# Kernel optimization log

Measured on AMD Instinct MI355X. Metric: run time of the kernel, lower is better.

## Reference

```python
import jax, jax.numpy as jnp
import numpy as np

B, S, D, H, DH = 2, 1024, 1024, 16, 64
SCALE = 1.0 / np.sqrt(DH)


def setup_inputs() -> dict:
    key = jax.random.key(0)
    ks = jax.random.split(key, 9)
    return {
        "x": jax.random.normal(ks[0], (B, S, D), jnp.float32),
        "qkv_w": jax.random.normal(ks[1], (3 * H * DH, D), jnp.float32) * 0.02,
        "out_w": jax.random.normal(ks[2], (D, H * DH), jnp.float32) * 0.02,
        "bias_p": jax.random.uniform(ks[3], (H, 1, 1), jnp.float32) * 2.0,
        "bias_a": jax.random.uniform(ks[4], (H, 1, 1), jnp.float32),
        "mlp_w1": jax.random.normal(ks[5], (H, 2 * H), jnp.float32) * 0.1,
        "mlp_b1": jnp.zeros((H,), jnp.float32),
        "mlp_w2": jax.random.normal(ks[6], (H, H), jnp.float32) * 0.1,
        "mlp_b2": jnp.zeros((H,), jnp.float32),
    }


def reference(x, qkv_w, out_w, bias_p, bias_a, mlp_w1, mlp_b1, mlp_w2, mlp_b2):
    # qkv projection: torch Linear => x @ W.T
    qkv = (x @ qkv_w.T).reshape(B, S, 3, H, DH)
    q = qkv[:, :, 0].transpose(0, 2, 1, 3)  # [B,H,S,DH]
    k = qkv[:, :, 1].transpose(0, 2, 1, 3)
    v = qkv[:, :, 2].transpose(0, 2, 1, 3)

    scores = jnp.einsum('bhqd,bhkd->bhqk', q, k) * SCALE  # [B,H,S,S]

    # Kerple additive bias: -p * log1p(a * |i-j|), per head
    p = jnp.clip(bias_p, 0.01)
    a = jnp.clip(bias_a, 0.01)
    pos = jnp.arange(S, dtype=jnp.float32)
    dist = jnp.abs(pos[None, :] - pos[:, None])  # [S,S]
    kb = -p * jnp.log1p(a * dist)  # [H,S,S]

    # DAPE refinement MLP over per-(i,j) head features
    z = jnp.concatenate(
        [scores, jnp.broadcast_to(kb[None], (B, H, S, S))], axis=1
    ).transpose(0, 2, 3, 1)  # [B,S,S,2H]
    hdn = jax.nn.gelu(z @ mlp_w1.T + mlp_b1, approximate=False)  # [B,S,S,H]
    refine = (hdn @ mlp_w2.T + mlp_b2).transpose(0, 3, 1, 2)  # [B,H,S,S]

    scores = scores + kb[None] + refine
    attn = jax.nn.softmax(scores, axis=-1)  # dropout is identity in eval

    out = jnp.einsum('bhqk,bhkd->bhqd', attn, v)  # [B,H,S,DH]
    out = out.transpose(0, 2, 1, 3).reshape(B, S, H * DH)
    return out @ out_w.T
```

## Files before the change

### kernel.cpp

```cpp
#include <hip/hip_runtime.h>
#include <math.h>

#define Bsz 2
#define Ssz 1024
#define Dsz 1024
#define Hn 16
#define DHsz 64
#define QKV3 3072
#define SCALE 0.125f

typedef __bf16 bf16;
typedef bf16 bf16x8 __attribute__((ext_vector_type(8)));
typedef bf16 bf16x4 __attribute__((ext_vector_type(4)));
typedef float f32x4 __attribute__((ext_vector_type(4)));

#define MFMA(a, b, c) __builtin_amdgcn_mfma_f32_16x16x32_bf16(a, b, c, 0, 0, 0)
#define LDT 72

#define SCSLAB(b, i, c) \
  ((size_t)(b) * 16777216 + (size_t)(i) * 16384 + (size_t)(c) * 4096)

__global__ void cast_all(const float* __restrict__ x, const float* __restrict__ qw,
                         const float* __restrict__ ow, bf16* __restrict__ xh,
                         bf16* __restrict__ wh, bf16* __restrict__ owh) {
  int idx = (blockIdx.x * 256 + threadIdx.x) * 4;
  const float* src;
  bf16* dst;
  int off = idx;
  if (idx < 2097152) {
    src = x; dst = xh;
  } else if (idx < 2097152 + 3145728) {
    src = qw; dst = wh; off = idx - 2097152;
  } else {
    src = ow; dst = owh; off = idx - (2097152 + 3145728);
  }
  float4 v = *(const float4*)(src + off);
  bf16x4 hv = {(bf16)v.x, (bf16)v.y, (bf16)v.z, (bf16)v.w};
  *(bf16x4*)(dst + off) = hv;
}

__global__ void tk_wfrag(const float* __restrict__ bias_p, const float* __restrict__ bias_a,
                         const float* __restrict__ w1, const float* __restrict__ b1,
                         const float* __restrict__ w2, float2* __restrict__ tk,
                         bf16* __restrict__ wf) {
  if (blockIdx.x == 128) {
    int lane = threadIdx.x;
    if (lane < 64) {
      int l15 = lane & 15, q8 = (lane >> 4) << 3;
      bf16x8 w1d, w2a;
#pragma unroll
      for (int e = 0; e < 8; ++e) {
        int k = q8 + e;
        if (k < 16) {
          w1d[e] = (bf16)w1[l15 * 32 + k];
        } else {
          float w = w1[l15 * 32 + k - 16];
          w1d[e] = (bf16)(w - (float)(bf16)w);
        }
        w2a[e] = (bf16)w2[l15 * 16 + (k & 15)];
      }
      *(bf16x8*)(wf + lane * 8) = w1d;
      *(bf16x8*)(wf + 512 + lane * 8) = w2a;
    }
    return;
  }
  int idx = blockIdx.x * 256 + threadIdx.x;
  int o = idx >> 4, n = idx & 15;
  int d = o - 1024; if (d < 0) d = -d; if (d > 1023) d = 1023;
  float fd = (float)d;
  float t1 = b1[n];
  float t2 = 0.f;
#pragma unroll
  for (int h = 0; h < 16; ++h) {
    float kb = -fmaxf(bias_p[h], 0.01f) * log1pf(fmaxf(bias_a[h], 0.01f) * fd);
    t1 += w1[n * 32 + 16 + h] * kb;
    if (h == n) t2 = kb;
  }
  tk[idx] = make_float2(t1, t2);
}

__global__ __launch_bounds__(256, 3) void k1_qkv(const bf16* __restrict__ A,
                                                 const bf16* __restrict__ B,
                                                 bf16* __restrict__ C) {
  __shared__ __align__(16) bf16 sA[128 * LDT];
  __shared__ __align__(16) bf16 sB[96 * LDT];
  const int tid = threadIdx.x;
  const int lane = tid & 63, wv = tid >> 6;
  const int wr = wv >> 1, wc = wv & 1;
  const int l15 = lane & 15, q8 = (lane >> 4) << 3, q4 = (lane >> 4) << 2;
  const int m0 = blockIdx.y * 128, n0 = blockIdx.x * 96;
  const int r0 = tid >> 3, c8 = (tid & 7) << 3;

  f32x4 acc[4][3];
#pragma unroll
  for (int t = 0; t < 4; ++t)
#pragma unroll
    for (int u = 0; u < 3; ++u)
#pragma unroll
      for (int r = 0; r < 4; ++r) acc[t][u][r] = 0.f;

  bf16x8 rA[4], rB[3];
#define K1_LOAD(kt)                                                         \
  {                                                                         \
    _Pragma("unroll") for (int c = 0; c < 4; ++c)                           \
      rA[c] = *(const bf16x8*)(A + (size_t)(m0 + c * 32 + r0) * Dsz + (kt) + c8);  \
    _Pragma("unroll") for (int c = 0; c < 3; ++c)                           \
      rB[c] = *(const bf16x8*)(B + (size_t)(n0 + c * 32 + r0) * Dsz + (kt) + c8);  \
  }

  K1_LOAD(0)
  for (int kt = 0; kt < Dsz; kt += 64) {
    __syncthreads();
#pragma unroll
    for (int c = 0; c < 4; ++c) *(bf16x8*)&sA[(c * 32 + r0) * LDT + c8] = rA[c];
#pragma unroll
    for (int c = 0; c < 3; ++c) *(bf16x8*)&sB[(c * 32 + r0) * LDT + c8] = rB[c];
    __syncthreads();
    if (kt + 64 < Dsz) K1_LOAD(kt + 64)
#pragma unroll
    for (int ks = 0; ks < 64; ks += 32) {
      bf16x8 fa[4], fb[3];
#pragma unroll
      for (int t = 0; t < 4; ++t)
        fa[t] = *(const bf16x8*)&sA[(wr * 64 + t * 16 + l15) * LDT + ks + q8];
#pragma unroll
      for (int u = 0; u < 3; ++u)
        fb[u] = *(const bf16x8*)&sB[(wc * 48 + u * 16 + l15) * LDT + ks + q8];
#pragma unroll
      for (int t = 0; t < 4; ++t)
#pragma unroll
        for (int u = 0; u < 3; ++u) acc[t][u] = MFMA(fa[t], fb[u], acc[t][u]);
    }
  }
#undef K1_LOAD

#define K1BST 104
  bf16* sBounce = sA;
#pragma unroll
  for (int t = 0; t < 4; ++t) {
    __syncthreads();
#pragma unroll
    for (int u = 0; u < 3; ++u) {
      int col = wc * 48 + u * 16 + l15;
#pragma unroll
      for (int r = 0; r < 4; ++r)
        sBounce[(wr * 16 + q4 + r) * K1BST + col] = (bf16)acc[t][u][r];
    }
    __syncthreads();
    int lr = tid >> 3;
    int grow = m0 + (lr < 16 ? t * 16 + lr : 64 + t * 16 + (lr - 16));
#pragma unroll
    for (int cg = 0; cg < 3; ++cg) {
      int cc = cg * 32 + (tid & 7) * 4;
      bf16x4 vv = *(const bf16x4*)&sBounce[lr * K1BST + cc];
      *(bf16x4*)(C + (size_t)grow * QKV3 + n0 + cc) = vv;
    }
  }
#undef K1BST
}

__global__ void pack_vt(const bf16* __restrict__ qkv, bf16* __restrict__ vt) {
  __shared__ __align__(16) bf16 T[64 * LDT];
  const int tid = threadIdx.x;
  const int bh = blockIdx.y, b = bh >> 4, h = bh & 15;
  const int j0 = blockIdx.x * 64;
#pragma unroll
  for (int c = 0; c < 2; ++c) {
    int lin = c * 256 + tid;
    int jr = lin >> 3, d8 = (lin & 7) << 3;
    bf16x8 v = *(const bf16x8*)(qkv + (size_t)(b * Ssz + j0 + jr) * QKV3 + 2048 + h * DHsz + d8);
#pragma unroll
    for (int e = 0; e < 8; ++e) T[(d8 + e) * LDT + jr] = v[e];
  }
  __syncthreads();
#pragma unroll
  for (int c = 0; c < 2; ++c) {
    int lin = c * 256 + tid;
    int d = lin >> 3, j8 = (lin & 7) << 3;
    bf16x8 o = *(const bf16x8*)&T[d * LDT + j8];
    *(bf16x8*)(vt + ((size_t)(b * Hn + h) * DHsz + d) * Ssz + j0 + j8) = o;
  }
}

__global__ __launch_bounds__(256, 3) void k2_qk(const bf16* __restrict__ qkv,
                                                bf16* __restrict__ scores) {
  __shared__ __align__(16) bf16 sA[128 * LDT], sB[128 * LDT];
  const int tid = threadIdx.x;
  const int lane = tid & 63, wv = tid >> 6;
  const int wr = wv >> 1, wc = wv & 1;
  const int l15 = lane & 15, q8 = (lane >> 4) << 3, q4 = (lane >> 4) << 2;
  const int z = blockIdx.z, b = z >> 4, h = z & 15;
  const int i0 = blockIdx.y * 128, j0 = blockIdx.x * 128;
  const bf16* Ab = qkv + (size_t)b * Ssz * QKV3 + h * DHsz;
  const bf16* Bb = Ab + Ssz;
  const int r0 = tid >> 3, c8 = (tid & 7) << 3;
#pragma unroll
  for (int c = 0; c < 4; ++c) {
    int row = c * 32 + r0;
    *(bf16x8*)&sA[row * LDT + c8] = *(const bf16x8*)(Ab + (size_t)(i0 + row) * QKV3 + c8);
    *(bf16x8*)&sB[row * LDT + c8] = *(const bf16x8*)(Bb + (size_t)(j0 + row) * QKV3 + c8);
  }
  __syncthreads();
  f32x4 acc[4][4];
#pragma unroll
  for (int t = 0; t < 4; ++t)
#pragma unroll
    for (int u = 0; u < 4; ++u)
#pragma unroll
      for (int r = 0; r < 4; ++r) acc[t][u][r] = 0.f;
#pragma unroll
  for (int ks = 0; ks < 64; ks += 32) {
    bf16x8 fa[4], fb[4];
#pragma unroll
    for (int t = 0; t < 4; ++t) fa[t] = *(const bf16x8*)&sA[(wr * 64 + t * 16 + l15) * LDT + ks + q8];
#pragma unroll
    for (int u = 0; u < 4; ++u) fb[u] = *(const bf16x8*)&sB[(wc * 64 + u * 16 + l15) * LDT + ks + q8];
#pragma unroll
    for (int t = 0; t < 4; ++t)
#pragma unroll
      for (int u = 0; u < 4; ++u) acc[t][u] = MFMA(fa[t], fb[u], acc[t][u]);
  }

#define K2BST 136
  bf16* sBounce = sA;
  const int chnk = j0 >> 8, jhalf = j0 & 128;
  bf16* base2 = scores + SCSLAB(b, 0, chnk) + h * 256 + jhalf;
#pragma unroll
  for (int t = 0; t < 4; ++t) {
    __syncthreads();
#pragma unroll
    for (int u = 0; u < 4; ++u) {
      int col = wc * 64 + u * 16 + l15;
#pragma unroll
      for (int r = 0; r < 4; ++r)
        sBounce[(wr * 16 + q4 + r) * K2BST + col] = (bf16)(acc[t][u][r] * SCALE);
    }
    __syncthreads();
#pragma unroll
    for (int hf = 0; hf < 2; ++hf) {
      int lr = hf * 16 + (tid >> 4);
      int cc = (tid & 15) * 8;
      bf16x8 vv = *(const bf16x8*)&sBounce[lr * K2BST + cc];
      int grow = i0 + (lr < 16 ? t * 16 + lr : 64 + t * 16 + (lr - 16));
      *(bf16x8*)(base2 + (size_t)grow * 16384 + cc) = vv;
    }
  }
#undef K2BST
}

__device__ __forceinline__ float gelu_fast(float x) {
  float z = fabsf(x) * 0.70710678118654752f;
  float t = __builtin_amdgcn_rcpf(fmaf(0.47047f, z, 1.0f));
  float poly = t * fmaf(t, fmaf(t, 0.7478556f, -0.0958798f), 0.3480242f);
  float erfa = 1.0f - poly * __expf(-z * z);
  float erfs = copysignf(erfa, x);
  return 0.5f * x * (1.0f + erfs);
}

#define SHS 264

__global__ __launch_bounds__(256, 8) void dape_softmax(bf16* scores,
                                                       const float2* __restrict__ tk,
                                                       const bf16* __restrict__ wf,
                                                       const float* __restrict__ b2,
                                                       float* __restrict__ sums) {
  const int c = blockIdx.x;
  const int i = blockIdx.y;
  const int b = blockIdx.z;
  const int tid = threadIdx.x;
  const int lane = tid & 63, wv = tid >> 6;
  const int l15 = lane & 15, q = lane >> 4;
  const int q8 = q << 3, q4 = q << 2;

  __shared__ bf16 sH[Hn][SHS];
  __shared__ __align__(16) bf16 hdnS[4][2][16][40];
  __shared__ float sumLDS[4][16];

  const bf16x8 w1d = *(const bf16x8*)(wf + lane * 8);
  const bf16x8 w2a = *(const bf16x8*)(wf + 512 + lane * 8);
  const float bias2 = b2[l15];

  if (lane < 32) {
    int row = lane >> 1, col = 16 + (lane & 1) * 8;
    *(bf16x8*)&hdnS[wv][0][row][col] = (bf16x8){};
    *(bf16x8*)&hdnS[wv][1][row][col] = (bf16x8){};
  }

  const int jw = wv * 64;
  bf16* slab = scores + SCSLAB(b, i, c);
#pragma unroll
  for (int t = 0; t < 2; ++t) {
    int h = t * 8 + (lane >> 3);
    int col = jw + (lane & 7) * 8;
    *(bf16x8*)&sH[h][col] = *(const bf16x8*)(slab + h * 256 + col);
  }

  const float2* tkp = tk + ((size_t)(c * 256 + jw + q4 - i + 1024) << 4) + l15;
  bf16* prow = slab + l15 * 256 + jw;
  float psum = 0.f;

#pragma unroll
  for (int jt = 0; jt < 4; ++jt) {
    const int j0c = jw + jt * 16;
    bf16x8 a1;
#pragma unroll
    for (int e = 0; e < 8; ++e) a1[e] = sH[(q8 + e) & 15][j0c + l15];
    float2 tkv[4];
#pragma unroll
    for (int r = 0; r < 4; ++r) tkv[r] = tkp[jt * 256 + r * 16];
    f32x4 c1 = {tkv[0].x, tkv[1].x, tkv[2].x, tkv[3].x};
    c1 = MFMA(a1, w1d, c1);
#pragma unroll
    for (int r = 0; r < 4; ++r) hdnS[wv][jt & 1][q4 + r][l15] = (bf16)gelu_fast(c1[r]);
    bf16x8 a2 = *(const bf16x8*)&hdnS[wv][jt & 1][l15][q8];
    f32x4 c2 = {bias2, bias2, bias2, bias2};
    c2 = MFMA(a2, w2a, c2);
    bf16x4 sc4 = *(const bf16x4*)&sH[l15][j0c + q4];
    f32x4 pv;
#pragma unroll
    for (int r = 0; r < 4; ++r) {
      float lg = (float)sc4[r] + tkv[r].y + c2[r];
      pv[r] = __expf(lg);
      psum += pv[r];
    }
    bf16x4 p4 = {(bf16)pv[0], (bf16)pv[1], (bf16)pv[2], (bf16)pv[3]};
    *(bf16x4*)(prow + jt * 16 + q4) = p4;
  }

  psum += __shfl_xor(psum, 16, 64);
  psum += __shfl_xor(psum, 32, 64);
  if (lane < 16) sumLDS[wv][lane] = psum;
  __syncthreads();
  if (tid < 16) {
    float tot = sumLDS[0][tid] + sumLDS[1][tid] + sumLDS[2][tid] + sumLDS[3][tid];
    sums[((((b << 10) + i) << 4) + tid) * 4 + c] = tot;
  }
}

__global__ __launch_bounds__(256, 6) void k4_av(const bf16* __restrict__ attn,
                                                const bf16* __restrict__ vt,
                                                const float* __restrict__ sums,
                                                bf16* __restrict__ aout) {
  __shared__ __align__(16) bf16 sA[64 * LDT], sB[64 * LDT];
  const int tid = threadIdx.x;
  const int lane = tid & 63, wv = tid >> 6;
  const int wr = wv >> 1, wc = wv & 1;
  const int l15 = lane & 15, q8 = (lane >> 4) << 3, q4 = (lane >> 4) << 2;
  const int i0 = blockIdx.x * 64, h = blockIdx.y, b = blockIdx.z;
  const bf16* Ab = attn + SCSLAB(b, i0, 0) + h * 256;
  const bf16* Bb = vt + (size_t)(b * Hn + h) * DHsz * Ssz;
  const int r0 = tid >> 3, c8 = (tid & 7) << 3;
  f32x4 acc[2][2];
#pragma unroll
  for (int t = 0; t < 2; ++t)
#pragma unroll
    for (int u = 0; u < 2; ++u)
#pragma unroll
      for (int r = 0; r < 4; ++r) acc[t][u][r] = 0.f;
  bf16x8 rA[2], rB[2];
#define K4_LOAD(kt)                                                          \
  {                                                                          \
    _Pragma("unroll") for (int c = 0; c < 2; ++c) {                          \
      int row = c * 32 + r0;                                                 \
      rA[c] = *(const bf16x8*)(Ab + (size_t)row * 16384 +                    \
                               (((kt) >> 8) * 4096) + ((kt) & 255) + c8);    \
      rB[c] = *(const bf16x8*)(Bb + ((size_t)row << 10) + (kt) + c8);        \
    }                                                                        \
  }
  K4_LOAD(0)
  for (int kt = 0; kt < Ssz; kt += 64) {
    __syncthreads();
#pragma unroll
    for (int c = 0; c < 2; ++c) {
      int row = c * 32 + r0;
      *(bf16x8*)&sA[row * LDT + c8] = rA[c];
      *(bf16x8*)&sB[row * LDT + c8] = rB[c];
    }
    __syncthreads();
    if (kt + 64 < Ssz) K4_LOAD(kt + 64)
#pragma unroll
    for (int ks = 0; ks < 64; ks += 32) {
      bf16x8 fa[2], fb[2];
#pragma unroll
      for (int t = 0; t < 2; ++t) fa[t] = *(const bf16x8*)&sA[(wr * 32 + t * 16 + l15) * LDT + ks + q8];
#pragma unroll
      for (int u = 0; u < 2; ++u) fb[u] = *(const bf16x8*)&sB[(wc * 32 + u * 16 + l15) * LDT + ks + q8];
#pragma unroll
      for (int t = 0; t < 2; ++t)
#pragma unroll
        for (int u = 0; u < 2; ++u) acc[t][u] = MFMA(fa[t], fb[u], acc[t][u]);
    }
  }
#undef K4_LOAD

  bf16* sBounce = sA;
  __syncthreads();
#pragma unroll
  for (int t = 0; t < 2; ++t)
#pragma unroll
    for (int r = 0; r < 4; ++r) {
      int lr = wr * 32 + t * 16 + q4 + r;
      int row = i0 + lr;
      f32x4 sv = *(const f32x4*)&sums[((((b << 10) + row) << 4) + h) * 4];
      float inv = 1.f / (sv[0] + sv[1] + sv[2] + sv[3]);
#pragma unroll
      for (int u = 0; u < 2; ++u)
        sBounce[lr * LDT + wc * 32 + u * 16 + l15] = (bf16)(acc[t][u][r] * inv);
    }
  __syncthreads();
#pragma unroll
  for (int r2 = 0; r2 < 2; ++r2) {
    int lr = r2 * 32 + (tid >> 3);
    int cc = (tid & 7) * 8;
    bf16x8 vv = *(const bf16x8*)&sBounce[lr * LDT + cc];
    *(bf16x8*)(aout + (size_t)(b * Ssz + i0 + lr) * Dsz + h * DHsz + cc) = vv;
  }
}

__global__ __launch_bounds__(256, 6) void k5_out(const bf16* __restrict__ A,
                                                 const bf16* __restrict__ B,
                                                 float* __restrict__ C) {
  __shared__ __align__(16) bf16 sA[64 * LDT], sB[64 * LDT];
  const int tid = threadIdx.x;
  const int lane = tid & 63, wv = tid >> 6;
  const int wr = wv >> 1, wc = wv & 1;
  const int l15 = lane & 15, q8 = (lane >> 4) << 3, q4 = (lane >> 4) << 2;
  const int m0 = blockIdx.y * 64, n0 = blockIdx.x * 64;
  const int r0 = tid >> 3, c8 = (tid & 7) << 3;
  f32x4 acc[2][2];
#pragma unroll
  for (int t = 0; t < 2; ++t)
#pragma unroll
    for (int u = 0; u < 2; ++u)
#pragma unroll
      for (int r = 0; r < 4; ++r) acc[t][u][r] = 0.f;
  bf16x8 rA[2], rB[2];
#define K5_LOAD(kt)                                                       \
  {                                                                       \
    _Pragma("unroll") for (int c = 0; c < 2; ++c) {                       \
      int row = c * 32 + r0;                                              \
      rA[c] = *(const bf16x8*)(A + (size_t)(m0 + row) * Dsz + (kt) + c8);   \
      rB[c] = *(const bf16x8*)(B + (size_t)(n0 + row) * Dsz + (kt) + c8);   \
    }                                                                     \
  }
  K5_LOAD(0)
  for (int kt = 0; kt < Dsz; kt += 64) {
    __syncthreads();
#pragma unroll
    for (int c = 0; c < 2; ++c) {
      int row = c * 32 + r0;
      *(bf16x8*)&sA[row * LDT + c8] = rA[c];
      *(bf16x8*)&sB[row * LDT + c8] = rB[c];
    }
    __syncthreads();
    if (kt + 64 < Dsz) K5_LOAD(kt + 64)
#pragma unroll
    for (int ks = 0; ks < 64; ks += 32) {
      bf16x8 fa[2], fb[2];
#pragma unroll
      for (int t = 0; t < 2; ++t) fa[t] = *(const bf16x8*)&sA[(wr * 32 + t * 16 + l15) * LDT + ks + q8];
#pragma unroll
      for (int u = 0; u < 2; ++u) fb[u] = *(const bf16x8*)&sB[(wc * 32 + u * 16 + l15) * LDT + ks + q8];
#pragma unroll
      for (int t = 0; t < 2; ++t)
#pragma unroll
        for (int u = 0; u < 2; ++u) acc[t][u] = MFMA(fa[t], fb[u], acc[t][u]);
    }
  }
#pragma unroll
  for (int t = 0; t < 2; ++t)
#pragma unroll
    for (int u = 0; u < 2; ++u) {
      int col = n0 + wc * 32 + u * 16 + l15;
#pragma unroll
      for (int r = 0; r < 4; ++r) {
        int row = m0 + wr * 32 + t * 16 + q4 + r;
        C[(size_t)row * Dsz + col] = acc[t][u][r];
      }
    }
#undef K5_LOAD
}

extern "C" void kernel_launch(void* const* d_in, const int* in_sizes, int n_in,
                              void* d_out, int out_size, void* d_ws, size_t ws_size,
                              hipStream_t stream) {
  const float* x      = (const float*)d_in[0];
  const float* qkv_w  = (const float*)d_in[1];
  const float* out_w  = (const float*)d_in[2];
  const float* bias_p = (const float*)d_in[3];
  const float* bias_a = (const float*)d_in[4];
  const float* w1     = (const float*)d_in[5];
  const float* b1     = (const float*)d_in[6];
  const float* w2     = (const float*)d_in[7];
  const float* b2     = (const float*)d_in[8];
  float* out = (float*)d_out;

  char* ws = (char*)d_ws;
  const size_t MB = 1ull << 20;
  bf16* ow_h   = (bf16*)(ws + 0 * MB);
  bf16* qkv_bf = (bf16*)(ws + 2 * MB);
  bf16* v_t    = (bf16*)(ws + 14 * MB);
  bf16* aout   = (bf16*)(ws + 18 * MB);
  float* sums  = (float*)(ws + 22 * MB + 65536);
  bf16* wf     = (bf16*)(ws + 22 * MB + 589824);
  float2* tk   = (float2*)(ws + 22 * MB + 655360);
  bf16* x_h    = (bf16*)(ws + 23 * MB);
  bf16* w_h    = (bf16*)(ws + 27 * MB);
  bf16* sc_bf  = (bf16*)(ws + 23 * MB);

  cast_all<<<6144, 256, 0, stream>>>(x, qkv_w, out_w, x_h, w_h, ow_h);
  tk_wfrag<<<129, 256, 0, stream>>>(bias_p, bias_a, w1, b1, w2, tk, wf);

  k1_qkv<<<dim3(QKV3 / 96, (Bsz * Ssz) / 128), 256, 0, stream>>>(x_h, w_h, qkv_bf);
  pack_vt<<<dim3(Ssz / 64, Bsz * Hn), 256, 0, stream>>>(qkv_bf, v_t);

  k2_qk<<<dim3(Ssz / 128, Ssz / 128, Bsz * Hn), 256, 0, stream>>>(qkv_bf, sc_bf);
  dape_softmax<<<dim3(4, Ssz, Bsz), 256, 0, stream>>>(sc_bf, tk, wf, b2, sums);
  k4_av<<<dim3(Ssz / 64, Hn, Bsz), 256, 0, stream>>>(sc_bf, v_t, sums, aout);

  k5_out<<<dim3(Dsz / 64, (Bsz * Ssz) / 64), 256, 0, stream>>>(aout, ow_h, out);
}
```

Measured before the change: 200.8 us.

## Merge four column-chunk blocks of dape_softmax into one 1024-thread block per row

The DAPE/softmax kernel now launches one 1024-thread block per (row, batch) covering all four 256-column chunks, not four 256-thread blocks. Row sums are reduced fully in-kernel and one scalar per (b,i,h) is written, so k4_av reads a single float instead of four partials. The per-wave hidden buffer loses its double buffering. This cuts block count and partial-sum traffic, at the cost of larger blocks with more LDS per block and a 1024-wide barrier, which may lower occupancy.

```diff
diff --git a/kernel.cpp b/kernel.cpp
--- a/kernel.cpp
+++ b/kernel.cpp
@@ -259,22 +259,22 @@
 
 #define SHS 264
 
-__global__ __launch_bounds__(256, 8) void dape_softmax(bf16* scores,
-                                                       const float2* __restrict__ tk,
-                                                       const bf16* __restrict__ wf,
-                                                       const float* __restrict__ b2,
-                                                       float* __restrict__ sums) {
-  const int c = blockIdx.x;
-  const int i = blockIdx.y;
-  const int b = blockIdx.z;
+__global__ __launch_bounds__(1024, 8) void dape_softmax(bf16* scores,
+                                                        const float2* __restrict__ tk,
+                                                        const bf16* __restrict__ wf,
+                                                        const float* __restrict__ b2,
+                                                        float* __restrict__ sums) {
+  const int i = blockIdx.x;
+  const int b = blockIdx.y;
   const int tid = threadIdx.x;
-  const int lane = tid & 63, wv = tid >> 6;
+  const int w = tid >> 6, lane = tid & 63;
+  const int c = w >> 2;
   const int l15 = lane & 15, q = lane >> 4;
   const int q8 = q << 3, q4 = q << 2;
 
-  __shared__ bf16 sH[Hn][SHS];
-  __shared__ __align__(16) bf16 hdnS[4][2][16][40];
-  __shared__ float sumLDS[4][16];
+  __shared__ bf16 sH[4][Hn][SHS];
+  __shared__ __align__(16) bf16 hdnS[16][16][40];
+  __shared__ float sumLDS[16][16];
 
   const bf16x8 w1d = *(const bf16x8*)(wf + lane * 8);
   const bf16x8 w2a = *(const bf16x8*)(wf + 512 + lane * 8);
@@ -282,17 +282,16 @@
 
   if (lane < 32) {
     int row = lane >> 1, col = 16 + (lane & 1) * 8;
-    *(bf16x8*)&hdnS[wv][0][row][col] = (bf16x8){};
-    *(bf16x8*)&hdnS[wv][1][row][col] = (bf16x8){};
-  }
-
-  const int jw = wv * 64;
+    *(bf16x8*)&hdnS[w][row][col] = (bf16x8){};
+  }
+
+  const int jw = (w & 3) * 64;
   bf16* slab = scores + SCSLAB(b, i, c);
 #pragma unroll
   for (int t = 0; t < 2; ++t) {
     int h = t * 8 + (lane >> 3);
     int col = jw + (lane & 7) * 8;
-    *(bf16x8*)&sH[h][col] = *(const bf16x8*)(slab + h * 256 + col);
+    *(bf16x8*)&sH[c][h][col] = *(const bf16x8*)(slab + h * 256 + col);
   }
 
   const float2* tkp = tk + ((size_t)(c * 256 + jw + q4 - i + 1024) << 4) + l15;
@@ -304,18 +303,18 @@
     const int j0c = jw + jt * 16;
     bf16x8 a1;
 #pragma unroll
-    for (int e = 0; e < 8; ++e) a1[e] = sH[(q8 + e) & 15][j0c + l15];
+    for (int e = 0; e < 8; ++e) a1[e] = sH[c][(q8 + e) & 15][j0c + l15];
     float2 tkv[4];
 #pragma unroll
     for (int r = 0; r < 4; ++r) tkv[r] = tkp[jt * 256 + r * 16];
     f32x4 c1 = {tkv[0].x, tkv[1].x, tkv[2].x, tkv[3].x};
     c1 = MFMA(a1, w1d, c1);
 #pragma unroll
-    for (int r = 0; r < 4; ++r) hdnS[wv][jt & 1][q4 + r][l15] = (bf16)gelu_fast(c1[r]);
-    bf16x8 a2 = *(const bf16x8*)&hdnS[wv][jt & 1][l15][q8];
+    for (int r = 0; r < 4; ++r) hdnS[w][q4 + r][l15] = (bf16)gelu_fast(c1[r]);
+    bf16x8 a2 = *(const bf16x8*)&hdnS[w][l15][q8];
     f32x4 c2 = {bias2, bias2, bias2, bias2};
     c2 = MFMA(a2, w2a, c2);
-    bf16x4 sc4 = *(const bf16x4*)&sH[l15][j0c + q4];
+    bf16x4 sc4 = *(const bf16x4*)&sH[c][l15][j0c + q4];
     f32x4 pv;
 #pragma unroll
     for (int r = 0; r < 4; ++r) {
@@ -329,11 +328,15 @@
 
   psum += __shfl_xor(psum, 16, 64);
   psum += __shfl_xor(psum, 32, 64);
-  if (lane < 16) sumLDS[wv][lane] = psum;
+  if (lane < 16) sumLDS[w][lane] = psum;
   __syncthreads();
   if (tid < 16) {
-    float tot = sumLDS[0][tid] + sumLDS[1][tid] + sumLDS[2][tid] + sumLDS[3][tid];
-    sums[((((b << 10) + i) << 4) + tid) * 4 + c] = tot;
+    int h = tid;
+    float s0 = ((sumLDS[0][h] + sumLDS[1][h]) + sumLDS[2][h]) + sumLDS[3][h];
+    float s1 = ((sumLDS[4][h] + sumLDS[5][h]) + sumLDS[6][h]) + sumLDS[7][h];
+    float s2 = ((sumLDS[8][h] + sumLDS[9][h]) + sumLDS[10][h]) + sumLDS[11][h];
+    float s3 = ((sumLDS[12][h] + sumLDS[13][h]) + sumLDS[14][h]) + sumLDS[15][h];
+    sums[(((b << 10) + i) << 4) + h] = ((s0 + s1) + s2) + s3;
   }
 }
 
@@ -401,8 +404,7 @@
     for (int r = 0; r < 4; ++r) {
       int lr = wr * 32 + t * 16 + q4 + r;
       int row = i0 + lr;
-      f32x4 sv = *(const f32x4*)&sums[((((b << 10) + row) << 4) + h) * 4];
-      float inv = 1.f / (sv[0] + sv[1] + sv[2] + sv[3]);
+      float inv = 1.f / sums[(((b << 10) + row) << 4) + h];
 #pragma unroll
       for (int u = 0; u < 2; ++u)
         sBounce[lr * LDT + wc * 32 + u * 16 + l15] = (bf16)(acc[t][u][r] * inv);
@@ -515,7 +517,7 @@
   pack_vt<<<dim3(Ssz / 64, Bsz * Hn), 256, 0, stream>>>(qkv_bf, v_t);
 
   k2_qk<<<dim3(Ssz / 128, Ssz / 128, Bsz * Hn), 256, 0, stream>>>(qkv_bf, sc_bf);
-  dape_softmax<<<dim3(4, Ssz, Bsz), 256, 0, stream>>>(sc_bf, tk, wf, b2, sums);
+  dape_softmax<<<dim3(Ssz, Bsz), 1024, 0, stream>>>(sc_bf, tk, wf, b2, sums);
   k4_av<<<dim3(Ssz / 64, Hn, Bsz), 256, 0, stream>>>(sc_bf, v_t, sums, aout);
 
   k5_out<<<dim3(Dsz / 64, (Bsz * Ssz) / 64), 256, 0, stream>>>(aout, ow_h, out);
```

New measurement: 198.1 us (median of 2 runs). About the same (-1.4%).
